# Optimization experiments

Measured on AMD Instinct MI355X. Metric: run time of the kernel, lower is better.

Reference implementation:

```python
import jax, jax.numpy as jnp
import numpy as np

# Static block sizes (2-layer neighbor-sampled blocks, fanout=10, 10k seed genes)
N_SRC1, N_DST1 = 1_210_000, 110_000
N_SRC2, N_DST2 = 110_000, 10_000
E1, E2 = 1_100_000, 100_000
IN_DIM, HID_DIM, OUT_DIM = 128, 256, 128


def setup_inputs() -> dict:
    key = jax.random.key(0)
    ks = jax.random.split(key, 12)
    feat = jax.random.normal(ks[0], (N_SRC1, IN_DIM), dtype=jnp.float32)
    src_idx1 = jax.random.randint(ks[1], (E1,), 0, N_SRC1)
    dst_idx1 = jax.random.randint(ks[2], (E1,), 0, N_DST1)
    src_idx2 = jax.random.randint(ks[3], (E2,), 0, N_SRC2)
    dst_idx2 = jax.random.randint(ks[4], (E2,), 0, N_DST2)
    s1 = 1.0 / np.sqrt(IN_DIM)
    s2 = 1.0 / np.sqrt(HID_DIM)
    W1 = jax.random.uniform(ks[5], (IN_DIM, HID_DIM), jnp.float32, -s1, s1)
    b1 = jnp.zeros((HID_DIM,), jnp.float32)
    attn1 = jax.random.uniform(ks[6], (HID_DIM, 1), jnp.float32, -s2, s2)
    W2 = jax.random.uniform(ks[7], (HID_DIM, OUT_DIM), jnp.float32, -s2, s2)
    b2 = jnp.zeros((OUT_DIM,), jnp.float32)
    s3 = 1.0 / np.sqrt(OUT_DIM)
    attn2 = jax.random.uniform(ks[8], (OUT_DIM, 1), jnp.float32, -s3, s3)
    return {"feat": feat, "W1": W1, "b1": b1, "attn1": attn1,
            "W2": W2, "b2": b2, "attn2": attn2,
            "src_idx1": src_idx1, "dst_idx1": dst_idx1,
            "src_idx2": src_idx2, "dst_idx2": dst_idx2}


def _gcn_gated_layer(h, src_idx, dst_idx, n_src, n_dst, W, b, attn_w):
    """DGL GraphConv(norm='both') on a block + sigmoid gene-attention gate."""
    ones = jnp.ones(src_idx.shape, jnp.float32)
    out_deg = jnp.clip(jax.ops.segment_sum(ones, src_idx, num_segments=n_src), 1.0)
    in_deg = jnp.clip(jax.ops.segment_sum(ones, dst_idx, num_segments=n_dst), 1.0)
    hs = h * jax.lax.rsqrt(out_deg)[:, None]            # src-side norm
    agg = jax.ops.segment_sum(hs[src_idx], dst_idx, num_segments=n_dst)
    hd = agg * jax.lax.rsqrt(in_deg)[:, None]           # dst-side norm
    hd = hd @ W + b                                     # GraphConv linear
    alpha = jax.nn.sigmoid(hd @ attn_w)                 # (n_dst, 1) gate
    return hd * alpha, alpha


def reference(feat, W1, b1, attn1, W2, b2, attn2,
              src_idx1, dst_idx1, src_idx2, dst_idx2):
    h, _ = _gcn_gated_layer(feat, src_idx1, dst_idx1, N_SRC1, N_DST1, W1, b1, attn1)
    h, alpha = _gcn_gated_layer(h, src_idx2, dst_idx2, N_SRC2, N_DST2, W2, b2, attn2)
    return h, alpha
```

## Files before the change

### kernel.cpp

```cpp
#include <hip/hip_runtime.h>
#include <cstddef>
#include <cstdint>

#define N_SRC1 1210000
#define N_DST1 110000
#define N_SRC2 110000
#define N_DST2 10000
#define E1 1100000
#define E2 100000
#define IN_DIM 128
#define HID_DIM 256
#define OUT_DIM 128

__global__ __launch_bounds__(256) void count_kernel(const int* __restrict__ src,
                                                    const int* __restrict__ dst,
                                                    float* __restrict__ outdeg,
                                                    int* __restrict__ cnt, int E) {
    int i = blockIdx.x * 256 + threadIdx.x;
    if (i < E) {
        unsafeAtomicAdd(&outdeg[src[i]], 1.0f);
        atomicAdd(&cnt[dst[i]], 1);
    }
}

__global__ __launch_bounds__(256) void rsqrt_kernel(float* __restrict__ p, int n) {
    int i = blockIdx.x * 256 + threadIdx.x;
    if (i < n) p[i] = rsqrtf(fmaxf(p[i], 1.0f));
}

__global__ __launch_bounds__(1024) void scan_kernel(const int* __restrict__ cnt,
                                                    int* __restrict__ offs,
                                                    int* __restrict__ cursor, int n) {
    __shared__ int smem[1024];
    __shared__ int running;
    if (threadIdx.x == 0) running = 0;
    __syncthreads();
    for (int base = 0; base < n; base += 1024) {
        int i = base + threadIdx.x;
        int v = (i < n) ? cnt[i] : 0;
        smem[threadIdx.x] = v;
        __syncthreads();
        #pragma unroll
        for (int off = 1; off < 1024; off <<= 1) {
            int t = (threadIdx.x >= off) ? smem[threadIdx.x - off] : 0;
            __syncthreads();
            smem[threadIdx.x] += t;
            __syncthreads();
        }
        int excl = smem[threadIdx.x] - v + running;
        if (i < n) { offs[i] = excl; cursor[i] = excl; }
        __syncthreads();
        if (threadIdx.x == 0) running += smem[1023];
        __syncthreads();
    }
    if (threadIdx.x == 0) offs[n] = running;
}

__global__ __launch_bounds__(256) void fill_kernel(const int* __restrict__ src,
                                                   const int* __restrict__ dst,
                                                   int* __restrict__ cursor,
                                                   int* __restrict__ elist, int E) {
    int i = blockIdx.x * 256 + threadIdx.x;
    if (i < E) {
        int pos = atomicAdd(&cursor[dst[i]], 1);
        elist[pos] = src[i];
    }
}

__global__ __launch_bounds__(256) void gather1_kernel(const float* __restrict__ feat,
                                                      const int* __restrict__ elist,
                                                      const int* __restrict__ offs,
                                                      const float* __restrict__ rs_out,
                                                      float* __restrict__ agg, int n_dst) {
    int d = blockIdx.x * 4 + (threadIdx.x >> 6);
    if (d >= n_dst) return;
    int lane = threadIdx.x & 63;
    int beg = offs[d], end = offs[d + 1];
    float2 acc = make_float2(0.f, 0.f);
    for (int j = beg; j < end; ++j) {
        int s = elist[j];
        float sc = rs_out[s];
        float2 v = ((const float2*)(feat + (size_t)s * IN_DIM))[lane];
        acc.x += v.x * sc;
        acc.y += v.y * sc;
    }
    float rin = rsqrtf(fmaxf((float)(end - beg), 1.f));
    acc.x *= rin; acc.y *= rin;
    ((float2*)(agg + (size_t)d * IN_DIM))[lane] = acc;
}

__global__ __launch_bounds__(256) void gather2_kernel(const float* __restrict__ h1,
                                                      const int* __restrict__ elist,
                                                      const int* __restrict__ offs,
                                                      const float* __restrict__ rs_out,
                                                      float* __restrict__ agg, int n_dst) {
    int d = blockIdx.x * 4 + (threadIdx.x >> 6);
    if (d >= n_dst) return;
    int lane = threadIdx.x & 63;
    int beg = offs[d], end = offs[d + 1];
    float4 acc = make_float4(0.f, 0.f, 0.f, 0.f);
    for (int j = beg; j < end; ++j) {
        int s = elist[j];
        float sc = rs_out[s];
        float4 v = ((const float4*)(h1 + (size_t)s * HID_DIM))[lane];
        acc.x += v.x * sc;
        acc.y += v.y * sc;
        acc.z += v.z * sc;
        acc.w += v.w * sc;
    }
    float rin = rsqrtf(fmaxf((float)(end - beg), 1.f));
    acc.x *= rin; acc.y *= rin; acc.z *= rin; acc.w *= rin;
    ((float4*)(agg + (size_t)d * HID_DIM))[lane] = acc;
}

__global__ __launch_bounds__(256) void gemm1_gate(const float* __restrict__ agg,
                                                  const float* __restrict__ W,
                                                  const float* __restrict__ bias,
                                                  const float* __restrict__ attn,
                                                  float* __restrict__ h1, int M) {
    __shared__ float As[32][IN_DIM + 4];
    __shared__ float Bs[32][HID_DIM];
    const int t = threadIdx.x;
    const int row0 = blockIdx.x * 32;
    const int col = t & 63;
    const int rbase = (t >> 6) * 8;

    #pragma unroll
    for (int i = 0; i < 4; ++i) {
        int idx = t + i * 256;
        int r = idx >> 5, c4 = idx & 31;
        int row = row0 + r;
        float4 v = make_float4(0.f, 0.f, 0.f, 0.f);
        if (row < M) v = ((const float4*)(agg + (size_t)row * IN_DIM))[c4];
        *(float4*)&As[r][c4 * 4] = v;
    }

    float4 acc[8];
    #pragma unroll
    for (int rr = 0; rr < 8; ++rr) acc[rr] = make_float4(0.f, 0.f, 0.f, 0.f);

    for (int kc = 0; kc < 4; ++kc) {
        __syncthreads();
        #pragma unroll
        for (int i = 0; i < 8; ++i) {
            int idx = t + i * 256;
            int kk = idx >> 6, c4 = idx & 63;
            *(float4*)&Bs[kk][c4 * 4] = ((const float4*)(W + (size_t)(kc * 32 + kk) * HID_DIM))[c4];
        }
        __syncthreads();
        #pragma unroll 2
        for (int k4 = 0; k4 < 8; ++k4) {
            int kk = k4 * 4;
            float4 b0 = *(float4*)&Bs[kk + 0][col * 4];
            float4 b1v = *(float4*)&Bs[kk + 1][col * 4];
            float4 b2v = *(float4*)&Bs[kk + 2][col * 4];
            float4 b3v = *(float4*)&Bs[kk + 3][col * 4];
            int ka = kc * 32 + kk;
            #pragma unroll
            for (int rr = 0; rr < 8; ++rr) {
                float4 a = *(const float4*)&As[rbase + rr][ka];
                acc[rr].x += a.x * b0.x + a.y * b1v.x + a.z * b2v.x + a.w * b3v.x;
                acc[rr].y += a.x * b0.y + a.y * b1v.y + a.z * b2v.y + a.w * b3v.y;
                acc[rr].z += a.x * b0.z + a.y * b1v.z + a.z * b2v.z + a.w * b3v.z;
                acc[rr].w += a.x * b0.w + a.y * b1v.w + a.z * b2v.w + a.w * b3v.w;
            }
        }
    }

    float4 bb = *(const float4*)&bias[col * 4];
    float4 at = *(const float4*)&attn[col * 4];
    #pragma unroll
    for (int rr = 0; rr < 8; ++rr) {
        int row = row0 + rbase + rr;
        float4 v = acc[rr];
        v.x += bb.x; v.y += bb.y; v.z += bb.z; v.w += bb.w;
        float p = v.x * at.x + v.y * at.y + v.z * at.z + v.w * at.w;
        p += __shfl_down(p, 32);
        p += __shfl_down(p, 16);
        p += __shfl_down(p, 8);
        p += __shfl_down(p, 4);
        p += __shfl_down(p, 2);
        p += __shfl_down(p, 1);
        p = __shfl(p, 0);
        float alpha = 1.f / (1.f + expf(-p));
        v.x *= alpha; v.y *= alpha; v.z *= alpha; v.w *= alpha;
        if (row < M) *(float4*)&h1[(size_t)row * HID_DIM + col * 4] = v;
    }
}

__global__ __launch_bounds__(256) void gemm2_gate(const float* __restrict__ agg,
                                                  const float* __restrict__ W,
                                                  const float* __restrict__ bias,
                                                  const float* __restrict__ attn,
                                                  float* __restrict__ out_h,
                                                  float* __restrict__ out_alpha, int M) {
    __shared__ float As[32][HID_DIM + 4];
    __shared__ float Bs[32][OUT_DIM];
    const int t = threadIdx.x;
    const int row0 = blockIdx.x * 32;
    const int col = t & 63;
    const int rbase = (t >> 6) * 8;

    #pragma unroll
    for (int i = 0; i < 8; ++i) {
        int idx = t + i * 256;
        int r = idx >> 6, c4 = idx & 63;
        int row = row0 + r;
        float4 v = make_float4(0.f, 0.f, 0.f, 0.f);
        if (row < M) v = ((const float4*)(agg + (size_t)row * HID_DIM))[c4];
        *(float4*)&As[r][c4 * 4] = v;
    }

    float2 acc[8];
    #pragma unroll
    for (int rr = 0; rr < 8; ++rr) acc[rr] = make_float2(0.f, 0.f);

    for (int kc = 0; kc < 8; ++kc) {
        __syncthreads();
        #pragma unroll
        for (int i = 0; i < 4; ++i) {
            int idx = t + i * 256;
            int kk = idx >> 5, c4 = idx & 31;
            *(float4*)&Bs[kk][c4 * 4] = ((const float4*)(W + (size_t)(kc * 32 + kk) * OUT_DIM))[c4];
        }
        __syncthreads();
        #pragma unroll
        for (int k4 = 0; k4 < 8; ++k4) {
            int kk = k4 * 4;
            float2 b0 = *(float2*)&Bs[kk + 0][col * 2];
            float2 b1v = *(float2*)&Bs[kk + 1][col * 2];
            float2 b2v = *(float2*)&Bs[kk + 2][col * 2];
            float2 b3v = *(float2*)&Bs[kk + 3][col * 2];
            int ka = kc * 32 + kk;
            #pragma unroll
            for (int rr = 0; rr < 8; ++rr) {
                float4 a = *(const float4*)&As[rbase + rr][ka];
                acc[rr].x += a.x * b0.x + a.y * b1v.x + a.z * b2v.x + a.w * b3v.x;
                acc[rr].y += a.x * b0.y + a.y * b1v.y + a.z * b2v.y + a.w * b3v.y;
            }
        }
    }

    float2 bb = *(const float2*)&bias[col * 2];
    float2 at = *(const float2*)&attn[col * 2];
    #pragma unroll
    for (int rr = 0; rr < 8; ++rr) {
        int row = row0 + rbase + rr;
        float2 v = acc[rr];
        v.x += bb.x; v.y += bb.y;
        float p = v.x * at.x + v.y * at.y;
        p += __shfl_down(p, 32);
        p += __shfl_down(p, 16);
        p += __shfl_down(p, 8);
        p += __shfl_down(p, 4);
        p += __shfl_down(p, 2);
        p += __shfl_down(p, 1);
        p = __shfl(p, 0);
        float alpha = 1.f / (1.f + expf(-p));
        v.x *= alpha; v.y *= alpha;
        if (row < M) {
            *(float2*)&out_h[(size_t)row * OUT_DIM + col * 2] = v;
            if (col == 0) out_alpha[row] = alpha;
        }
    }
}

extern "C" void kernel_launch(void* const* d_in, const int* in_sizes, int n_in,
                              void* d_out, int out_size, void* d_ws, size_t ws_size,
                              hipStream_t stream) {
    const float* feat  = (const float*)d_in[0];
    const float* W1    = (const float*)d_in[1];
    const float* b1    = (const float*)d_in[2];
    const float* attn1 = (const float*)d_in[3];
    const float* W2    = (const float*)d_in[4];
    const float* b2    = (const float*)d_in[5];
    const float* attn2 = (const float*)d_in[6];
    const int* src1 = (const int*)d_in[7];
    const int* dst1 = (const int*)d_in[8];
    const int* src2 = (const int*)d_in[9];
    const int* dst2 = (const int*)d_in[10];
    float* out = (float*)d_out;

    float* ws = (float*)d_ws;
    float* outdeg1 = ws;
    float* outdeg2 = outdeg1 + N_SRC1;
    int*   cnt1    = (int*)(outdeg2 + N_SRC2);
    int*   cnt2    = cnt1 + N_DST1;
    int*   offs1   = cnt2 + N_DST2;
    int*   cursor1 = offs1 + N_DST1 + 1;
    int*   offs2   = cursor1 + N_DST1;
    int*   cursor2 = offs2 + N_DST2 + 1;
    int*   elist1  = cursor2 + N_DST2;
    int*   elist2  = elist1 + E1;
    float* agg1    = (float*)(elist2 + E2);
    float* agg2    = agg1 + (size_t)N_DST1 * IN_DIM;
    float* h1      = agg2 + (size_t)N_DST2 * HID_DIM;

    const size_t zero_bytes = ((size_t)N_SRC1 + N_SRC2 + N_DST1 + N_DST2) * 4;
    hipMemsetAsync(d_ws, 0, zero_bytes, stream);

    count_kernel<<<(E1 + 255) / 256, 256, 0, stream>>>(src1, dst1, outdeg1, cnt1, E1);
    count_kernel<<<(E2 + 255) / 256, 256, 0, stream>>>(src2, dst2, outdeg2, cnt2, E2);
    rsqrt_kernel<<<(N_SRC1 + N_SRC2 + 255) / 256, 256, 0, stream>>>(outdeg1, N_SRC1 + N_SRC2);

    scan_kernel<<<1, 1024, 0, stream>>>(cnt1, offs1, cursor1, N_DST1);
    scan_kernel<<<1, 1024, 0, stream>>>(cnt2, offs2, cursor2, N_DST2);
    fill_kernel<<<(E1 + 255) / 256, 256, 0, stream>>>(src1, dst1, cursor1, elist1, E1);
    fill_kernel<<<(E2 + 255) / 256, 256, 0, stream>>>(src2, dst2, cursor2, elist2, E2);

    gather1_kernel<<<(N_DST1 + 3) / 4, 256, 0, stream>>>(feat, elist1, offs1, outdeg1, agg1, N_DST1);
    gemm1_gate<<<(N_DST1 + 31) / 32, 256, 0, stream>>>(agg1, W1, b1, attn1, h1, N_DST1);
    gather2_kernel<<<(N_DST2 + 3) / 4, 256, 0, stream>>>(h1, elist2, offs2, outdeg2, agg2, N_DST2);
    gemm2_gate<<<(N_DST2 + 31) / 32, 256, 0, stream>>>(agg2, W2, b2, attn2,
                                                       out, out + (size_t)N_DST2 * OUT_DIM, N_DST2);
}
```

Baseline: 1.446 ms.

## Replace single-block prefix scan with multi-block three-phase scan

The CSR offset scan previously ran in one 1024-thread block looping serially over all destination counts. It is now split into per-block partial scans, a single-block scan of block sums, and an add-back pass that also initializes the cursors. This spreads the scan across many CUs to cut the serialized barrier chain, at the cost of extra kernel launches and a small extra workspace region for block sums.

```diff
diff --git a/kernel.cpp b/kernel.cpp
--- a/kernel.cpp
+++ b/kernel.cpp
@@ -28,32 +28,51 @@
     if (i < n) p[i] = rsqrtf(fmaxf(p[i], 1.0f));
 }
 
-__global__ __launch_bounds__(1024) void scan_kernel(const int* __restrict__ cnt,
-                                                    int* __restrict__ offs,
-                                                    int* __restrict__ cursor, int n) {
+__global__ __launch_bounds__(1024) void scan_part(const int* __restrict__ cnt,
+                                                  int* __restrict__ offs,
+                                                  int* __restrict__ bsum, int n) {
     __shared__ int smem[1024];
-    __shared__ int running;
-    if (threadIdx.x == 0) running = 0;
+    int i = blockIdx.x * 1024 + threadIdx.x;
+    int v = (i < n) ? cnt[i] : 0;
+    smem[threadIdx.x] = v;
     __syncthreads();
-    for (int base = 0; base < n; base += 1024) {
-        int i = base + threadIdx.x;
-        int v = (i < n) ? cnt[i] : 0;
-        smem[threadIdx.x] = v;
-        __syncthreads();
-        #pragma unroll
-        for (int off = 1; off < 1024; off <<= 1) {
-            int t = (threadIdx.x >= off) ? smem[threadIdx.x - off] : 0;
-            __syncthreads();
-            smem[threadIdx.x] += t;
-            __syncthreads();
-        }
-        int excl = smem[threadIdx.x] - v + running;
-        if (i < n) { offs[i] = excl; cursor[i] = excl; }
-        __syncthreads();
-        if (threadIdx.x == 0) running += smem[1023];
-        __syncthreads();
-    }
-    if (threadIdx.x == 0) offs[n] = running;
+    #pragma unroll
+    for (int off = 1; off < 1024; off <<= 1) {
+        int t = (threadIdx.x >= off) ? smem[threadIdx.x - off] : 0;
+        __syncthreads();
+        smem[threadIdx.x] += t;
+        __syncthreads();
+    }
+    if (i < n) offs[i] = smem[threadIdx.x] - v;
+    if (threadIdx.x == 1023) bsum[blockIdx.x] = smem[1023];
+}
+
+__global__ __launch_bounds__(1024) void scan_bsum(int* __restrict__ bsum,
+                                                  int* __restrict__ offs_end, int nb) {
+    __shared__ int smem[1024];
+    int v = (threadIdx.x < nb) ? bsum[threadIdx.x] : 0;
+    smem[threadIdx.x] = v;
+    __syncthreads();
+    #pragma unroll
+    for (int off = 1; off < 1024; off <<= 1) {
+        int t = (threadIdx.x >= off) ? smem[threadIdx.x - off] : 0;
+        __syncthreads();
+        smem[threadIdx.x] += t;
+        __syncthreads();
+    }
+    if (threadIdx.x < nb) bsum[threadIdx.x] = smem[threadIdx.x] - v;
+    if (threadIdx.x == nb - 1) *offs_end = smem[threadIdx.x];
+}
+
+__global__ __launch_bounds__(1024) void scan_add(int* __restrict__ offs,
+                                                 int* __restrict__ cursor,
+                                                 const int* __restrict__ bsum, int n) {
+    int i = blockIdx.x * 1024 + threadIdx.x;
+    if (i < n) {
+        int o = offs[i] + bsum[blockIdx.x];
+        offs[i] = o;
+        cursor[i] = o;
+    }
 }
 
 __global__ __launch_bounds__(256) void fill_kernel(const int* __restrict__ src,
@@ -295,6 +314,8 @@
     float* agg1    = (float*)(elist2 + E2);
     float* agg2    = agg1 + (size_t)N_DST1 * IN_DIM;
     float* h1      = agg2 + (size_t)N_DST2 * HID_DIM;
+    int*   bsum1   = (int*)(h1 + (size_t)N_DST1 * HID_DIM);
+    int*   bsum2   = bsum1 + 128;
 
     const size_t zero_bytes = ((size_t)N_SRC1 + N_SRC2 + N_DST1 + N_DST2) * 4;
     hipMemsetAsync(d_ws, 0, zero_bytes, stream);
@@ -303,8 +324,15 @@
     count_kernel<<<(E2 + 255) / 256, 256, 0, stream>>>(src2, dst2, outdeg2, cnt2, E2);
     rsqrt_kernel<<<(N_SRC1 + N_SRC2 + 255) / 256, 256, 0, stream>>>(outdeg1, N_SRC1 + N_SRC2);
 
-    scan_kernel<<<1, 1024, 0, stream>>>(cnt1, offs1, cursor1, N_DST1);
-    scan_kernel<<<1, 1024, 0, stream>>>(cnt2, offs2, cursor2, N_DST2);
+    const int nb1 = (N_DST1 + 1023) / 1024;
+    const int nb2 = (N_DST2 + 1023) / 1024;
+    scan_part<<<nb1, 1024, 0, stream>>>(cnt1, offs1, bsum1, N_DST1);
+    scan_bsum<<<1, 1024, 0, stream>>>(bsum1, offs1 + N_DST1, nb1);
+    scan_add<<<nb1, 1024, 0, stream>>>(offs1, cursor1, bsum1, N_DST1);
+    scan_part<<<nb2, 1024, 0, stream>>>(cnt2, offs2, bsum2, N_DST2);
+    scan_bsum<<<1, 1024, 0, stream>>>(bsum2, offs2 + N_DST2, nb2);
+    scan_add<<<nb2, 1024, 0, stream>>>(offs2, cursor2, bsum2, N_DST2);
+
     fill_kernel<<<(E1 + 255) / 256, 256, 0, stream>>>(src1, dst1, cursor1, elist1, E1);
     fill_kernel<<<(E2 + 255) / 256, 256, 0, stream>>>(src2, dst2, cursor2, elist2, E2);
 
```

Result: faster. 1.247 ms (-13.8%).
